# Performance work log

Hardware: AMD Instinct MI355X
Metric: run time of the kernel (lower is better)

The kernel has to match this reference:

```python
import jax, jax.numpy as jnp
import numpy as np

L, D, FF, H, S, B, W = 4, 768, 3072, 12, 4096, 4, 128


def setup_inputs() -> dict:
    key = jax.random.key(0)
    ks = jax.random.split(key, 8)
    w_ = lambda k, shape: jax.random.normal(k, shape, jnp.float32) * 0.02
    return {
        "x": jax.random.normal(ks[0], (B, S, D), jnp.float32),
        "Wq": w_(ks[1], (L, D, D)), "bq": jnp.zeros((L, D), jnp.float32),
        "Wk": w_(ks[2], (L, D, D)), "bk": jnp.zeros((L, D), jnp.float32),
        "Wv": w_(ks[3], (L, D, D)), "bv": jnp.zeros((L, D), jnp.float32),
        "W1": w_(ks[4], (L, D, FF)), "b1": jnp.zeros((L, FF), jnp.float32),
        "W2": w_(ks[5], (L, FF, D)), "b2": jnp.zeros((L, D), jnp.float32),
        "g1": jnp.ones((L, D), jnp.float32), "beta1": jnp.zeros((L, D), jnp.float32),
        "g2": jnp.ones((L, D), jnp.float32), "beta2": jnp.zeros((L, D), jnp.float32),
        "n_heads": H,
        "window": W,
    }


def _layernorm(x, g, b, eps=1e-5):
    m = jnp.mean(x, axis=-1, keepdims=True)
    v = jnp.mean(jnp.square(x - m), axis=-1, keepdims=True)
    return (x - m) * jax.lax.rsqrt(v + eps) * g + b


def _sliding_attn(x, Wq, bq, Wk, bk, Wv, bv, n_heads, w):
    # Longformer 'sliding_chunks' self-attention, one-sided window w (band 2w+1).
    b_, s_, d_ = x.shape
    hd = d_ // n_heads
    nc = s_ // w  # number of query chunks of size w

    def proj(Wm, bm):
        p = x @ Wm + bm
        return p.reshape(b_, s_, n_heads, hd).transpose(0, 2, 1, 3)  # [B,H,S,hd]

    q = proj(Wq, bq) / jnp.sqrt(jnp.asarray(hd, x.dtype))
    k = proj(Wk, bk)
    v = proj(Wv, bv)

    # pad keys/values by one window each side so every query chunk sees 3w keys
    kp = jnp.pad(k, ((0, 0), (0, 0), (w, w), (0, 0)))
    vp = jnp.pad(v, ((0, 0), (0, 0), (w, w), (0, 0)))
    idx = jnp.arange(nc)[:, None] * w + jnp.arange(3 * w)[None, :]  # [nc, 3w]
    kb = kp[:, :, idx]  # [B,H,nc,3w,hd]
    vb = vp[:, :, idx]
    qc = q.reshape(b_, n_heads, nc, w, hd)

    scores = jnp.einsum('bhcqd,bhckd->bhcqk', qc, kb)  # [B,H,nc,w,3w]

    # band + boundary mask: key pos = c*w + kj - w, query pos = c*w + qi
    c = jnp.arange(nc)[:, None, None]
    qi = jnp.arange(w)[None, :, None]
    kj = jnp.arange(3 * w)[None, None, :]
    rel = kj - qi - w
    kpos = c * w + kj - w
    mask = (jnp.abs(rel) <= w) & (kpos >= 0) & (kpos < s_)  # [nc,w,3w]

    scores = jnp.where(mask[None, None], scores, -jnp.inf)
    attn = jax.nn.softmax(scores, axis=-1)
    out = jnp.einsum('bhcqk,bhckd->bhcqd', attn, vb)  # [B,H,nc,w,hd]
    return out.reshape(b_, n_heads, s_, hd).transpose(0, 2, 1, 3).reshape(b_, s_, d_)


def reference(x, Wq, bq, Wk, bk, Wv, bv, W1, b1, W2, b2, g1, beta1, g2, beta2,
              n_heads, window):
    n_layers = Wq.shape[0]
    for l in range(n_layers):
        attn = _sliding_attn(x, Wq[l], bq[l], Wk[l], bk[l], Wv[l], bv[l],
                             n_heads, window)
        x = _layernorm(x + attn, g1[l], beta1[l])
        h = jnp.maximum(x @ W1[l] + b1[l], 0.0) @ W2[l] + b2[l]
        x = _layernorm(x + h, g2[l], beta2[l])
    return x
```

## Files before the change

kernel.cpp:

```cpp
#include <hip/hip_runtime.h>
#include <hip/hip_bf16.h>
#include <type_traits>

#define LAYERS 4
#define D      768
#define FF     3072
#define NH     12
#define HD     64
#define SEQ    4096
#define BATCH  4
#define WIN    128
#define NC     (SEQ / WIN)
#define NTOK   (BATCH * SEQ)

using bf16 = __hip_bfloat16;
typedef short short8 __attribute__((ext_vector_type(8)));
typedef short short4v __attribute__((ext_vector_type(4)));
typedef float floatx4 __attribute__((ext_vector_type(4)));

__device__ __forceinline__ float b2f(unsigned short u) {
    return __uint_as_float(((unsigned)u) << 16);
}
__device__ __forceinline__ short f2bs(float f) {
    union { bf16 h; short s; } u; u.h = __float2bfloat16(f); return u.s;
}
__device__ __forceinline__ void st_cvt(float* p, float v) { *p = v; }
__device__ __forceinline__ void st_cvt(bf16* p, float v) { *p = __float2bfloat16(v); }

__device__ __forceinline__ void gl_lds16(const void* g, void* l) {
    __builtin_amdgcn_global_load_lds(
        (const __attribute__((address_space(1))) void*)g,
        (__attribute__((address_space(3))) void*)l, 16, 0, 0);
}

__global__ __launch_bounds__(256)
void cvt_f32_bf16(const float* __restrict__ src, bf16* __restrict__ dst)
{
    const int i = (blockIdx.x * 256 + threadIdx.x) * 8;
    const float4 a0 = *(const float4*)(src + i);
    const float4 a1 = *(const float4*)(src + i + 4);
    short8 p = { f2bs(a0.x), f2bs(a0.y), f2bs(a0.z), f2bs(a0.w),
                 f2bs(a1.x), f2bs(a1.y), f2bs(a1.z), f2bs(a1.w) };
    *(short8*)((short*)dst + i) = p;
}

__global__ __launch_bounds__(256)
void transpose_cvt(const float* __restrict__ src, bf16* __restrict__ dst, int K, int N)
{
    __shared__ float t[32][33];
    const int n0 = blockIdx.x * 32, k0 = blockIdx.y * 32;
    const int tx = threadIdx.x & 31, ty = threadIdx.x >> 5;
    #pragma unroll
    for (int r = 0; r < 4; ++r)
        t[ty + 8 * r][tx] = src[(size_t)(k0 + ty + 8 * r) * N + n0 + tx];
    __syncthreads();
    #pragma unroll
    for (int r = 0; r < 4; ++r)
        dst[(size_t)(n0 + ty + 8 * r) * K + k0 + tx] = __float2bfloat16(t[tx][ty + 8 * r]);
}

template<int RELU, int OMODE, typename TC>
__global__ __launch_bounds__(256)
void mfma_gemm_bf(const bf16* __restrict__ A, const bf16* __restrict__ Wt,
                  const float* __restrict__ bias, TC* __restrict__ C,
                  int M, int N, int K, float scale)
{
    __shared__ __align__(16) short As[128 * 32];
    __shared__ __align__(16) short Bs[128 * 32];
    const int tid  = threadIdx.x;
    const int lane = tid & 63;
    const int wave = tid >> 6;
    const int quad = lane >> 4, l16 = lane & 15;
    const int mw = (wave >> 1) * 64, nw = (wave & 1) * 64;
    const int row0 = blockIdx.x * 128;
    const int col0 = blockIdx.y * 128;

    const unsigned short* Ag = (const unsigned short*)A;
    const unsigned short* Bg = (const unsigned short*)Wt;
    const int sr = lane >> 2;
    const int sc = (lane & 3) * 8;

    floatx4 acc[4][4];
    const floatx4 zero = {0.f, 0.f, 0.f, 0.f};
    #pragma unroll
    for (int i = 0; i < 4; ++i)
        #pragma unroll
        for (int j = 0; j < 4; ++j) acc[i][j] = zero;

    const size_t abase = (size_t)row0 * K;
    const size_t bbase = (size_t)col0 * K;

    for (int k0 = 0; k0 < K; k0 += 32) {
        __syncthreads();
        #pragma unroll
        for (int e = 0; e < 2; ++e) {
            const int seg = wave * 2 + e;
            const int r = seg * 16 + sr;
            gl_lds16(Ag + abase + (size_t)r * K + k0 + sc, &As[seg * 512]);
            gl_lds16(Bg + bbase + (size_t)r * K + k0 + sc, &Bs[seg * 512]);
        }
        __syncthreads();
        short8 af[4], bfr[4];
        #pragma unroll
        for (int i = 0; i < 4; ++i)
            af[i] = *(const short8*)&As[(mw + 16 * i + l16) * 32 + quad * 8];
        #pragma unroll
        for (int j = 0; j < 4; ++j)
            bfr[j] = *(const short8*)&Bs[(nw + 16 * j + l16) * 32 + quad * 8];
        #pragma unroll
        for (int i = 0; i < 4; ++i)
            #pragma unroll
            for (int j = 0; j < 4; ++j)
                acc[i][j] = __builtin_amdgcn_mfma_f32_16x16x32_bf16(af[i], bfr[j], acc[i][j], 0, 0, 0);
    }
    #pragma unroll
    for (int j = 0; j < 4; ++j) {
        const int c = col0 + nw + 16 * j + l16;
        const float bv = bias[c];
        #pragma unroll
        for (int i = 0; i < 4; ++i) {
            const int rr0 = row0 + mw + 16 * i + quad * 4;
            if constexpr (OMODE == 2) {
                short4v pack;
                #pragma unroll
                for (int r = 0; r < 4; ++r)
                    pack[r] = f2bs((acc[i][j][r] + bv) * scale);
                const int b_ = rr0 >> 12, s_ = rr0 & (SEQ - 1);
                const int h_ = c >> 6, d_ = c & (HD - 1);
                *(short4v*)&C[(((size_t)(b_ * NH + h_)) * HD + d_) * SEQ + s_] = pack;
            } else {
                #pragma unroll
                for (int r = 0; r < 4; ++r) {
                    float v = acc[i][j][r] + bv;
                    if (RELU) v = fmaxf(v, 0.f);
                    v *= scale;
                    const int rr = rr0 + r;
                    if constexpr (OMODE == 1) {
                        const int b_ = rr >> 12, s_ = rr & (SEQ - 1);
                        const int h_ = c >> 6, d_ = c & (HD - 1);
                        st_cvt(&C[(((size_t)(b_ * NH + h_)) * SEQ + s_) * HD + d_], v);
                    } else {
                        st_cvt(&C[(size_t)rr * N + c], v);
                    }
                }
            }
        }
    }
}

template<int RELU, int OMODE, typename TA, typename TC>
__global__ __launch_bounds__(256)
void mfma_gemm(const TA* __restrict__ A, const float* __restrict__ Wf,
               const float* __restrict__ bias,
               TC* __restrict__ C, int M, int N, int K, float scale)
{
    __shared__ __align__(16) short As[128][40];
    __shared__ __align__(16) short Bs[128][40];
    const int row0 = blockIdx.x * 128;
    const int col0 = blockIdx.y * 128;
    const int tid  = threadIdx.x;
    const int lane = tid & 63;
    const int wave = tid >> 6;
    const int quad = lane >> 4, l16 = lane & 15;
    const int mw = (wave >> 1) * 64, nw = (wave & 1) * 64;

    const int ar = tid >> 1;
    const int ah = (tid & 1) * 16;
    const int bn = tid & 127;
    const int bk = (tid >> 7) * 8;

    floatx4 acc[4][4];
    const floatx4 zero = {0.f, 0.f, 0.f, 0.f};
    #pragma unroll
    for (int i = 0; i < 4; ++i)
        #pragma unroll
        for (int j = 0; j < 4; ++j) acc[i][j] = zero;

    for (int k0 = 0; k0 < K; k0 += 32) {
        __syncthreads();
        if constexpr (std::is_same<TA, float>::value) {
            const float* ap = A + (size_t)(row0 + ar) * K + k0 + ah;
            float4 a0 = *(const float4*)(ap);
            float4 a1 = *(const float4*)(ap + 4);
            float4 a2 = *(const float4*)(ap + 8);
            float4 a3 = *(const float4*)(ap + 12);
            short8 p0 = { f2bs(a0.x), f2bs(a0.y), f2bs(a0.z), f2bs(a0.w),
                          f2bs(a1.x), f2bs(a1.y), f2bs(a1.z), f2bs(a1.w) };
            short8 p1 = { f2bs(a2.x), f2bs(a2.y), f2bs(a2.z), f2bs(a2.w),
                          f2bs(a3.x), f2bs(a3.y), f2bs(a3.z), f2bs(a3.w) };
            *(short8*)&As[ar][ah]     = p0;
            *(short8*)&As[ar][ah + 8] = p1;
        } else {
            const short* ap = (const short*)A + (size_t)(row0 + ar) * K + k0 + ah;
            *(short8*)&As[ar][ah]     = *(const short8*)(ap);
            *(short8*)&As[ar][ah + 8] = *(const short8*)(ap + 8);
        }
        #pragma unroll
        for (int kc = 0; kc < 2; ++kc) {
            const int kk = bk + kc * 16;
            short tmp[8];
            #pragma unroll
            for (int e = 0; e < 8; ++e)
                tmp[e] = f2bs(Wf[(size_t)(k0 + kk + e) * N + col0 + bn]);
            *(short8*)&Bs[bn][kk] = *(short8*)tmp;
        }
        __syncthreads();
        short8 af[4], bfr[4];
        #pragma unroll
        for (int i = 0; i < 4; ++i)
            af[i] = *(const short8*)&As[mw + 16 * i + l16][quad * 8];
        #pragma unroll
        for (int j = 0; j < 4; ++j)
            bfr[j] = *(const short8*)&Bs[nw + 16 * j + l16][quad * 8];
        #pragma unroll
        for (int i = 0; i < 4; ++i)
            #pragma unroll
            for (int j = 0; j < 4; ++j)
                acc[i][j] = __builtin_amdgcn_mfma_f32_16x16x32_bf16(af[i], bfr[j], acc[i][j], 0, 0, 0);
    }
    #pragma unroll
    for (int j = 0; j < 4; ++j) {
        const int c = col0 + nw + 16 * j + l16;
        const float bv = bias[c];
        #pragma unroll
        for (int i = 0; i < 4; ++i) {
            const int rr0 = row0 + mw + 16 * i + quad * 4;
            if constexpr (OMODE == 2) {
                short4v pack;
                #pragma unroll
                for (int r = 0; r < 4; ++r)
                    pack[r] = f2bs((acc[i][j][r] + bv) * scale);
                const int b_ = rr0 >> 12, s_ = rr0 & (SEQ - 1);
                const int h_ = c >> 6, d_ = c & (HD - 1);
                *(short4v*)&C[(((size_t)(b_ * NH + h_)) * HD + d_) * SEQ + s_] = pack;
            } else {
                #pragma unroll
                for (int r = 0; r < 4; ++r) {
                    float v = acc[i][j][r] + bv;
                    if (RELU) v = fmaxf(v, 0.f);
                    v *= scale;
                    const int rr = rr0 + r;
                    if constexpr (OMODE == 1) {
                        const int b_ = rr >> 12, s_ = rr & (SEQ - 1);
                        const int h_ = c >> 6, d_ = c & (HD - 1);
                        st_cvt(&C[(((size_t)(b_ * NH + h_)) * SEQ + s_) * HD + d_], v);
                    } else {
                        st_cvt(&C[(size_t)rr * N + c], v);
                    }
                }
            }
        }
    }
}

__global__ __launch_bounds__(256, 2)
void attn_mfma_kernel(const bf16* __restrict__ q, const bf16* __restrict__ k,
                      const bf16* __restrict__ v, bf16* __restrict__ out)
{
    __shared__ __align__(16) short Qs[128][72];
    __shared__ __align__(16) short Ks[64][72];
    __shared__ __align__(16) short Vs[64][72];
    __shared__ __align__(16) short Ps[4][32][72];

    const int c = blockIdx.x, h = blockIdx.y, b = blockIdx.z;
    const int tid = threadIdx.x;
    const int wave = tid >> 6, lane = tid & 63;
    const int quad = lane >> 4, l16 = lane & 15;
    const int qbase = wave * 32;

    const unsigned short* qg = (const unsigned short*)q + ((size_t)(b * NH + h)) * SEQ * HD;
    const unsigned short* kg = (const unsigned short*)k + ((size_t)(b * NH + h)) * SEQ * HD;
    const unsigned short* vg = (const unsigned short*)v + ((size_t)(b * NH + h)) * HD * SEQ;

    #pragma unroll
    for (int e = 0; e < 4; ++e) {
        const int idx = tid + e * 256;
        const int row = idx >> 3, d0 = (idx & 7) * 8;
        *(uint4*)&Qs[row][d0] = *(const uint4*)(qg + (size_t)(c * WIN + row) * HD + d0);
    }

    floatx4 O[2][4];
    const floatx4 zero = {0.f, 0.f, 0.f, 0.f};
    float m_i[2][4], l_i[2][4];
    #pragma unroll
    for (int i = 0; i < 2; ++i)
        #pragma unroll
        for (int r = 0; r < 4; ++r) { m_i[i][r] = -1e30f; l_i[i][r] = 0.f; }
    #pragma unroll
    for (int i = 0; i < 2; ++i)
        #pragma unroll
        for (int dj = 0; dj < 4; ++dj) O[i][dj] = zero;

    for (int sl = 0; sl < 6; ++sl) {
        const int s0 = sl * 64;
        const int kpos0 = c * WIN - WIN + s0;
        if (kpos0 < 0 || kpos0 >= SEQ) continue;
        __syncthreads();
        #pragma unroll
        for (int e = 0; e < 2; ++e) {
            const int idx = tid + e * 256;
            const int row = idx >> 3, d0 = (idx & 7) * 8;
            *(uint4*)&Ks[row][d0] = *(const uint4*)(kg + (size_t)(kpos0 + row) * HD + d0);
            *(uint4*)&Vs[row][d0] = *(const uint4*)(vg + (size_t)row * SEQ + kpos0 + d0);
        }
        __syncthreads();
        short8 aq[2][2], bk2[4][2];
        #pragma unroll
        for (int i = 0; i < 2; ++i)
            #pragma unroll
            for (int hh = 0; hh < 2; ++hh)
                aq[i][hh] = *(const short8*)&Qs[qbase + 16 * i + l16][hh * 32 + quad * 8];
        #pragma unroll
        for (int j = 0; j < 4; ++j)
            #pragma unroll
            for (int hh = 0; hh < 2; ++hh)
                bk2[j][hh] = *(const short8*)&Ks[16 * j + l16][hh * 32 + quad * 8];
        floatx4 sc[2][4];
        #pragma unroll
        for (int i = 0; i < 2; ++i)
            #pragma unroll
            for (int j = 0; j < 4; ++j) {
                floatx4 t = __builtin_amdgcn_mfma_f32_16x16x32_bf16(aq[i][0], bk2[j][0], zero, 0, 0, 0);
                sc[i][j]  = __builtin_amdgcn_mfma_f32_16x16x32_bf16(aq[i][1], bk2[j][1], t, 0, 0, 0);
            }
        #pragma unroll
        for (int i = 0; i < 2; ++i) {
            #pragma unroll
            for (int r = 0; r < 4; ++r) {
                const int qq = qbase + 16 * i + quad * 4 + r;
                float sv[4];
                float mx = -1e30f;
                #pragma unroll
                for (int j = 0; j < 4; ++j) {
                    const int kj = s0 + 16 * j + l16;
                    const bool ok = (kj >= qq) && (kj <= qq + 2 * WIN);
                    const float s = ok ? sc[i][j][r] : -1e30f;
                    sv[j] = s;
                    mx = fmaxf(mx, s);
                }
                mx = fmaxf(mx, __shfl_xor(mx, 1));
                mx = fmaxf(mx, __shfl_xor(mx, 2));
                mx = fmaxf(mx, __shfl_xor(mx, 4));
                mx = fmaxf(mx, __shfl_xor(mx, 8));
                const float mn = fmaxf(m_i[i][r], mx);
                const float corr = __expf(m_i[i][r] - mn);
                m_i[i][r] = mn;
                float ps = 0.f;
                #pragma unroll
                for (int j = 0; j < 4; ++j) {
                    const float p = (sv[j] > -0.9e30f) ? __expf(sv[j] - mn) : 0.f;
                    ps += p;
                    Ps[wave][16 * i + quad * 4 + r][16 * j + l16] = f2bs(p);
                }
                ps += __shfl_xor(ps, 1);
                ps += __shfl_xor(ps, 2);
                ps += __shfl_xor(ps, 4);
                ps += __shfl_xor(ps, 8);
                l_i[i][r] = l_i[i][r] * corr + ps;
                #pragma unroll
                for (int dj = 0; dj < 4; ++dj) O[i][dj][r] *= corr;
            }
        }
        short8 ap[2][2], bv2[4][2];
        #pragma unroll
        for (int i = 0; i < 2; ++i)
            #pragma unroll
            for (int hh = 0; hh < 2; ++hh)
                ap[i][hh] = *(const short8*)&Ps[wave][16 * i + l16][hh * 32 + quad * 8];
        #pragma unroll
        for (int dj = 0; dj < 4; ++dj)
            #pragma unroll
            for (int hh = 0; hh < 2; ++hh)
                bv2[dj][hh] = *(const short8*)&Vs[16 * dj + l16][hh * 32 + quad * 8];
        #pragma unroll
        for (int i = 0; i < 2; ++i)
            #pragma unroll
            for (int dj = 0; dj < 4; ++dj) {
                O[i][dj] = __builtin_amdgcn_mfma_f32_16x16x32_bf16(ap[i][0], bv2[dj][0], O[i][dj], 0, 0, 0);
                O[i][dj] = __builtin_amdgcn_mfma_f32_16x16x32_bf16(ap[i][1], bv2[dj][1], O[i][dj], 0, 0, 0);
            }
    }
    bf16* og = out + ((size_t)b * SEQ + c * WIN) * D + h * HD;
    #pragma unroll
    for (int i = 0; i < 2; ++i) {
        #pragma unroll
        for (int r = 0; r < 4; ++r) {
            const float inv = 1.f / l_i[i][r];
            const int qq = qbase + 16 * i + quad * 4 + r;
            #pragma unroll
            for (int dj = 0; dj < 4; ++dj)
                og[(size_t)qq * D + 16 * dj + l16] = __float2bfloat16(O[i][dj][r] * inv);
        }
    }
}

template<int WBF>
__global__ __launch_bounds__(256)
void add_ln_kernel(const float* __restrict__ xin, const bf16* __restrict__ h,
                   float* __restrict__ xout, bf16* __restrict__ xbf,
                   const float* __restrict__ g, const float* __restrict__ beta)
{
    const int row = blockIdx.x;
    __shared__ float buf[D];
    __shared__ float wsum[4], wsum2[4];
    const float* xr = xin + (size_t)row * D;
    const bf16* hr = h + (size_t)row * D;
    float s = 0.f, s2 = 0.f;
    #pragma unroll
    for (int e = 0; e < 3; ++e) {
        const int i = threadIdx.x + e * 256;
        const float t = xr[i] + __bfloat162float(hr[i]);
        buf[i] = t;
        s += t; s2 += t * t;
    }
    #pragma unroll
    for (int off = 32; off > 0; off >>= 1) {
        s  += __shfl_down(s, off);
        s2 += __shfl_down(s2, off);
    }
    const int wid = threadIdx.x >> 6, lane = threadIdx.x & 63;
    if (lane == 0) { wsum[wid] = s; wsum2[wid] = s2; }
    __syncthreads();
    if (threadIdx.x == 0) {
        const float S  = wsum[0] + wsum[1] + wsum[2] + wsum[3];
        const float S2 = wsum2[0] + wsum2[1] + wsum2[2] + wsum2[3];
        const float mean = S * (1.f / D);
        const float var  = S2 * (1.f / D) - mean * mean;
        wsum[0]  = mean;
        wsum2[0] = rsqrtf(var + 1e-5f);
    }
    __syncthreads();
    const float mean = wsum[0], inv = wsum2[0];
    #pragma unroll
    for (int e = 0; e < 3; ++e) {
        const int i = threadIdx.x + e * 256;
        const float val = (buf[i] - mean) * inv * g[i] + beta[i];
        xout[(size_t)row * D + i] = val;
        if constexpr (WBF)
            xbf[(size_t)row * D + i] = __float2bfloat16(val);
    }
}

static void run_fast(const float* x0,
                     const float* Wq, const float* bq, const float* Wk, const float* bk,
                     const float* Wv, const float* bv, const float* W1, const float* b1,
                     const float* W2, const float* b2, const float* g1, const float* be1,
                     const float* g2, const float* be2, float* out,
                     bf16* qb, bf16* kb, bf16* vb, bf16* hb, bf16* mid, bf16* h2,
                     bf16* wt, bf16* xbf, hipStream_t stream)
{
    const dim3 gD(NTOK / 128, D / 128);
    const dim3 gF(NTOK / 128, FF / 128);
    const dim3 ga(NC, NH, BATCH);
    const size_t DDm = (size_t)D * D, DFFm = (size_t)D * FF;

    cvt_f32_bf16<<<NTOK * D / 2048, 256, 0, stream>>>(x0, xbf);
    for (int l = 0; l < LAYERS; ++l) {
        const float* xin = (l == 0) ? x0 : out;
        transpose_cvt<<<dim3(D / 32, D / 32), 256, 0, stream>>>(
            Wq + (size_t)l * DDm, wt, D, D);
        transpose_cvt<<<dim3(D / 32, D / 32), 256, 0, stream>>>(
            Wk + (size_t)l * DDm, wt + DDm, D, D);
        transpose_cvt<<<dim3(D / 32, D / 32), 256, 0, stream>>>(
            Wv + (size_t)l * DDm, wt + 2 * DDm, D, D);
        transpose_cvt<<<dim3(FF / 32, D / 32), 256, 0, stream>>>(
            W1 + (size_t)l * DFFm, wt + 3 * DDm, D, FF);
        transpose_cvt<<<dim3(D / 32, FF / 32), 256, 0, stream>>>(
            W2 + (size_t)l * DFFm, wt + 3 * DDm + DFFm, FF, D);

        mfma_gemm_bf<0, 1, bf16><<<gD, 256, 0, stream>>>(
            xbf, wt, bq + (size_t)l * D, qb, NTOK, D, D, 0.125f);
        mfma_gemm_bf<0, 1, bf16><<<gD, 256, 0, stream>>>(
            xbf, wt + DDm, bk + (size_t)l * D, kb, NTOK, D, D, 1.0f);
        mfma_gemm_bf<0, 2, bf16><<<gD, 256, 0, stream>>>(
            xbf, wt + 2 * DDm, bv + (size_t)l * D, vb, NTOK, D, D, 1.0f);
        attn_mfma_kernel<<<ga, 256, 0, stream>>>(qb, kb, vb, hb);
        add_ln_kernel<1><<<NTOK, 256, 0, stream>>>(xin, hb, out, xbf,
            g1 + (size_t)l * D, be1 + (size_t)l * D);
        mfma_gemm_bf<1, 0, bf16><<<gF, 256, 0, stream>>>(
            xbf, wt + 3 * DDm, b1 + (size_t)l * FF, mid, NTOK, FF, D, 1.0f);
        mfma_gemm_bf<0, 0, bf16><<<gD, 256, 0, stream>>>(
            mid, wt + 3 * DDm + DFFm, b2 + (size_t)l * D, h2, NTOK, D, FF, 1.0f);
        add_ln_kernel<1><<<NTOK, 256, 0, stream>>>(out, h2, out, xbf,
            g2 + (size_t)l * D, be2 + (size_t)l * D);
    }
}

static void run_fallback(const float* x0,
                         const float* Wq, const float* bq, const float* Wk, const float* bk,
                         const float* Wv, const float* bv, const float* W1, const float* b1,
                         const float* W2, const float* b2, const float* g1, const float* be1,
                         const float* g2, const float* be2, float* out,
                         bf16* qb, bf16* kb, bf16* vb, bf16* hb, bf16* mid, bf16* h2,
                         hipStream_t stream)
{
    const dim3 gD(NTOK / 128, D / 128);
    const dim3 gF(NTOK / 128, FF / 128);
    const dim3 ga(NC, NH, BATCH);
    for (int l = 0; l < LAYERS; ++l) {
        const float* xin = (l == 0) ? x0 : out;
        mfma_gemm<0, 1, float, bf16><<<gD, 256, 0, stream>>>(
            xin, Wq + (size_t)l * D * D, bq + (size_t)l * D, qb, NTOK, D, D, 0.125f);
        mfma_gemm<0, 1, float, bf16><<<gD, 256, 0, stream>>>(
            xin, Wk + (size_t)l * D * D, bk + (size_t)l * D, kb, NTOK, D, D, 1.0f);
        mfma_gemm<0, 2, float, bf16><<<gD, 256, 0, stream>>>(
            xin, Wv + (size_t)l * D * D, bv + (size_t)l * D, vb, NTOK, D, D, 1.0f);
        attn_mfma_kernel<<<ga, 256, 0, stream>>>(qb, kb, vb, hb);
        add_ln_kernel<0><<<NTOK, 256, 0, stream>>>(xin, hb, out, nullptr,
            g1 + (size_t)l * D, be1 + (size_t)l * D);
        mfma_gemm<1, 0, float, bf16><<<gF, 256, 0, stream>>>(
            out, W1 + (size_t)l * D * FF, b1 + (size_t)l * FF, mid, NTOK, FF, D, 1.0f);
        mfma_gemm<0, 0, bf16, bf16><<<gD, 256, 0, stream>>>(
            mid, W2 + (size_t)l * FF * D, b2 + (size_t)l * D, h2, NTOK, D, FF, 1.0f);
        add_ln_kernel<0><<<NTOK, 256, 0, stream>>>(out, h2, out, nullptr,
            g2 + (size_t)l * D, be2 + (size_t)l * D);
    }
}

extern "C" void kernel_launch(void* const* d_in, const int* in_sizes, int n_in,
                              void* d_out, int out_size, void* d_ws, size_t ws_size,
                              hipStream_t stream)
{
    const float* x0  = (const float*)d_in[0];
    const float* Wq  = (const float*)d_in[1];
    const float* bq  = (const float*)d_in[2];
    const float* Wk  = (const float*)d_in[3];
    const float* bk  = (const float*)d_in[4];
    const float* Wv  = (const float*)d_in[5];
    const float* bv  = (const float*)d_in[6];
    const float* W1  = (const float*)d_in[7];
    const float* b1  = (const float*)d_in[8];
    const float* W2  = (const float*)d_in[9];
    const float* b2  = (const float*)d_in[10];
    const float* g1  = (const float*)d_in[11];
    const float* be1 = (const float*)d_in[12];
    const float* g2  = (const float*)d_in[13];
    const float* be2 = (const float*)d_in[14];
    float* out = (float*)d_out;

    const size_t QE = (size_t)BATCH * NH * SEQ * HD;
    const size_t LW = (size_t)3 * D * D + 2 * (size_t)D * FF;
    bf16* qb  = (bf16*)d_ws;
    bf16* kb  = qb + QE;
    bf16* vb  = kb + QE;
    bf16* hb  = vb + QE;
    bf16* mid = qb;
    bf16* h2  = qb + 4 * QE;
    bf16* wt  = qb + 5 * QE;
    bf16* xbf = wt + LW;
    const bool fast = ws_size >= (6 * QE + LW) * sizeof(bf16);

    if (fast) {
        run_fast(x0, Wq, bq, Wk, bk, Wv, bv, W1, b1, W2, b2, g1, be1, g2, be2,
                 out, qb, kb, vb, hb, mid, h2, wt, xbf, stream);
    } else {
        run_fallback(x0, Wq, bq, Wk, bk, Wv, bv, W1, b1, W2, b2, g1, be1, g2, be2,
                     out, qb, kb, vb, hb, mid, h2, stream);
    }
}
```

Measured before the change: 1.898 ms.

## Add 256x256 eight-wave pipelined GEMM with fused QKV projection

Replaces the 128x128 four-wave GEMMs with a new 256x256-tile, 512-thread kernel. It uses direct global-to-LDS loads into a swizzled, double-buffered 128KB LDS layout, interleaves MFMA and load phases with explicit barriers, waitcnts and priority hints, and remaps blocks for cache locality. The Q, K and V projections are merged into one launch with N=2304, and each output slice is routed with its own bias, scale and layout. The aim is higher MFMA utilisation and fewer launches, at the cost of a large LDS footprint per block and a fragile hand-tuned schedule.

```diff
diff --git a/kernel.cpp b/kernel.cpp
--- a/kernel.cpp
+++ b/kernel.cpp
@@ -33,6 +33,14 @@
         (__attribute__((address_space(3))) void*)l, 16, 0, 0);
 }
 
+#define SB0   __builtin_amdgcn_sched_barrier(0)
+#define BAR   __builtin_amdgcn_s_barrier()
+#define LGKM0 asm volatile("s_waitcnt lgkmcnt(0)" ::: "memory")
+#define VM4   asm volatile("s_waitcnt vmcnt(4)" ::: "memory")
+#define VM0   asm volatile("s_waitcnt vmcnt(0)" ::: "memory")
+#define SP1   __builtin_amdgcn_s_setprio(1)
+#define SP0   __builtin_amdgcn_s_setprio(0)
+
 __global__ __launch_bounds__(256)
 void cvt_f32_bf16(const float* __restrict__ src, bf16* __restrict__ dst)
 {
@@ -59,10 +67,175 @@
         dst[(size_t)(n0 + ty + 8 * r) * K + k0 + tx] = __float2bfloat16(t[tx][ty + 8 * r]);
 }
 
-template<int RELU, int OMODE, typename TC>
+template<int OMODE, int RELU>
+__global__ __launch_bounds__(512, 2)
+void gemm8(const bf16* __restrict__ A, const bf16* __restrict__ Wt,
+           const float* __restrict__ b0, const float* __restrict__ b1p,
+           const float* __restrict__ b2p, bf16* __restrict__ C,
+           int K, int N)
+{
+    extern __shared__ char ldsc[];
+    const int tid  = threadIdx.x;
+    const int lane = tid & 63;
+    const int wave = tid >> 6;
+    const int quad = lane >> 4, l16 = lane & 15;
+    const int wm = wave >> 2, wn = wave & 3;
+
+    const int bx  = blockIdx.x;
+    const int bxs = (bx & 7) * 8 + (bx >> 3);
+    const int row0 = bxs * 256;
+    const int col0 = blockIdx.y * 256;
+
+    const int lin0 = wave * 1024 + lane * 16;
+    const int lin1 = 8192 + wave * 1024 + lane * 16;
+    const int rl0 = lin0 >> 7, rl1 = lin1 >> 7;
+    const int so0 = (lin0 & 127) ^ ((rl0 & 7) << 4);
+    const int so1 = (lin1 & 127) ^ ((rl1 & 7) << 4);
+    const char* agl0 = (const char*)A  + 2 * ((size_t)(row0 + rl0) * K) + so0;
+    const char* agl1 = (const char*)A  + 2 * ((size_t)(row0 + rl1) * K) + so1;
+    const char* bgl0 = (const char*)Wt + 2 * ((size_t)(col0 + rl0) * K) + so0;
+    const char* bgl1 = (const char*)Wt + 2 * ((size_t)(col0 + rl1) * K) + so1;
+    const size_t hstr = (size_t)128 * K * 2;
+
+#define STA(d,h,kt) do { \
+    gl_lds16(agl0 + ((h) ? hstr : 0) + (size_t)(kt) * 128, ldsc + ((d)*2+(h))*16384 + lin0); \
+    gl_lds16(agl1 + ((h) ? hstr : 0) + (size_t)(kt) * 128, ldsc + ((d)*2+(h))*16384 + lin1); } while (0)
+#define STB(d,h,kt) do { \
+    gl_lds16(bgl0 + ((h) ? hstr : 0) + (size_t)(kt) * 128, ldsc + 65536 + ((d)*2+(h))*16384 + lin0); \
+    gl_lds16(bgl1 + ((h) ? hstr : 0) + (size_t)(kt) * 128, ldsc + 65536 + ((d)*2+(h))*16384 + lin1); } while (0)
+
+    const int arow  = wm * 64 + l16;
+    const int abase = arow * 128;
+    const int sA    = (arow & 7) << 4;
+    const int aof0  = (quad * 16) ^ sA;
+    const int aof1  = (64 + quad * 16) ^ sA;
+    const int brow  = wn * 32 + l16;
+    const int bbase = brow * 128;
+    const int sB    = (brow & 7) << 4;
+    const int bof0  = (quad * 16) ^ sB;
+    const int bof1  = (64 + quad * 16) ^ sB;
+
+    short8 af[4][2], bf0[2][2], bf1[2][2];
+    floatx4 acc[2][2][4][2];
+    const floatx4 zero = {0.f, 0.f, 0.f, 0.f};
+    #pragma unroll
+    for (int a = 0; a < 2; ++a)
+        #pragma unroll
+        for (int b = 0; b < 2; ++b)
+            #pragma unroll
+            for (int m = 0; m < 4; ++m)
+                #pragma unroll
+                for (int n = 0; n < 2; ++n) acc[a][b][m][n] = zero;
+
+#define LDA(slot) do { const char* ab_ = ldsc + (slot)*16384 + abase; \
+    _Pragma("unroll") for (int m_ = 0; m_ < 4; ++m_) { \
+        af[m_][0] = *(const short8*)(ab_ + m_*2048 + aof0); \
+        af[m_][1] = *(const short8*)(ab_ + m_*2048 + aof1); } } while (0)
+#define LDB(slot, BF) do { const char* bb_ = ldsc + 65536 + (slot)*16384 + bbase; \
+    _Pragma("unroll") for (int n_ = 0; n_ < 2; ++n_) { \
+        BF[n_][0] = *(const short8*)(bb_ + n_*2048 + bof0); \
+        BF[n_][1] = *(const short8*)(bb_ + n_*2048 + bof1); } } while (0)
+#define MM(mh, nh, BF) do { \
+    _Pragma("unroll") for (int m_ = 0; m_ < 4; ++m_) \
+    _Pragma("unroll") for (int n_ = 0; n_ < 2; ++n_) { \
+        acc[mh][nh][m_][n_] = __builtin_amdgcn_mfma_f32_16x16x32_bf16(af[m_][0], BF[n_][0], acc[mh][nh][m_][n_], 0, 0, 0); \
+        acc[mh][nh][m_][n_] = __builtin_amdgcn_mfma_f32_16x16x32_bf16(af[m_][1], BF[n_][1], acc[mh][nh][m_][n_], 0, 0, 0); } } while (0)
+
+    const int nkt   = K >> 6;
+    const int niter = K >> 7;
+
+    STA(0,0,0); STB(0,0,0); STA(0,1,0); STB(0,1,0);
+    STA(1,0,1); STB(1,0,1);
+    VM4; SB0; BAR;
+
+    for (int i = 0; i < niter; ++i) {
+        const int k1 = 2*i + 1;
+        const int k2 = (2*i + 2 < nkt) ? 2*i + 2 : nkt - 1;
+        const int k3 = (2*i + 3 < nkt) ? 2*i + 3 : nkt - 1;
+        LDA(0); LDB(0, bf0); STA(1,1,k1); SB0; BAR; LGKM0; SB0;
+        SP1; MM(0,0,bf0); SP0; SB0; BAR;
+        LDB(1, bf1); STB(1,1,k1); SB0; BAR; LGKM0; SB0;
+        SP1; MM(0,1,bf1); SP0; SB0; BAR;
+        LDA(1); STA(0,0,k2); SB0; BAR; LGKM0; SB0;
+        SP1; MM(1,0,bf0); SP0; SB0; BAR;
+        STB(0,0,k2); SB0; BAR; LGKM0; SB0;
+        SP1; MM(1,1,bf1); SP0; VM4; SB0; BAR;
+        LDA(2); LDB(2, bf0); STA(0,1,k2); SB0; BAR; LGKM0; SB0;
+        SP1; MM(0,0,bf0); SP0; SB0; BAR;
+        LDB(3, bf1); STB(0,1,k2); SB0; BAR; LGKM0; SB0;
+        SP1; MM(0,1,bf1); SP0; SB0; BAR;
+        LDA(3); STA(1,0,k3); SB0; BAR; LGKM0; SB0;
+        SP1; MM(1,0,bf0); SP0; SB0; BAR;
+        STB(1,0,k3); SB0; BAR; LGKM0; SB0;
+        SP1; MM(1,1,bf1); SP0; VM4; SB0; BAR;
+    }
+    VM0;
+
+#undef STA
+#undef STB
+#undef LDA
+#undef LDB
+#undef MM
+
+    constexpr size_t QEc = (size_t)BATCH * NH * SEQ * HD;
+    int sel = 0;
+    const float* bptr = b0;
+    float scl = 1.0f;
+    int ccb = col0;
+    if constexpr (OMODE == 3) {
+        sel  = blockIdx.y / 3;
+        bptr = (sel == 0) ? b0 : (sel == 1) ? b1p : b2p;
+        scl  = (sel == 0) ? 0.125f : 1.0f;
+        ccb  = col0 - sel * 768;
+    }
+    #pragma unroll
+    for (int mh = 0; mh < 2; ++mh)
+    #pragma unroll
+    for (int nh = 0; nh < 2; ++nh)
+    #pragma unroll
+    for (int n = 0; n < 2; ++n) {
+        const int c  = ccb + nh * 128 + wn * 32 + n * 16 + l16;
+        const float bvv = bptr[c];
+        #pragma unroll
+        for (int m = 0; m < 4; ++m) {
+            const int rr0 = row0 + mh * 128 + wm * 64 + m * 16 + quad * 4;
+            if constexpr (OMODE == 3) {
+                if (sel == 2) {
+                    short4v pack;
+                    #pragma unroll
+                    for (int r = 0; r < 4; ++r)
+                        pack[r] = f2bs(acc[mh][nh][m][n][r] + bvv);
+                    const int b_ = rr0 >> 12, s_ = rr0 & (SEQ - 1);
+                    const int h_ = c >> 6, d_ = c & (HD - 1);
+                    bf16* Cv = C + 2 * QEc;
+                    *(short4v*)&Cv[(((size_t)(b_ * NH + h_)) * HD + d_) * SEQ + s_] = pack;
+                } else {
+                    bf16* Cq = C + (size_t)sel * QEc;
+                    #pragma unroll
+                    for (int r = 0; r < 4; ++r) {
+                        const float v = (acc[mh][nh][m][n][r] + bvv) * scl;
+                        const int rr = rr0 + r;
+                        const int b_ = rr >> 12, s_ = rr & (SEQ - 1);
+                        const int h_ = c >> 6, d_ = c & (HD - 1);
+                        Cq[(((size_t)(b_ * NH + h_)) * SEQ + s_) * HD + d_] = __float2bfloat16(v);
+                    }
+                }
+            } else {
+                #pragma unroll
+                for (int r = 0; r < 4; ++r) {
+                    float v = acc[mh][nh][m][n][r] + bvv;
+                    if (RELU) v = fmaxf(v, 0.f);
+                    C[(size_t)(rr0 + r) * N + c] = __float2bfloat16(v);
+                }
+            }
+        }
+    }
+}
+
+template<int RELU, int OMODE>
 __global__ __launch_bounds__(256)
 void mfma_gemm_bf(const bf16* __restrict__ A, const bf16* __restrict__ Wt,
-                  const float* __restrict__ bias, TC* __restrict__ C,
+                  const float* __restrict__ bias, bf16* __restrict__ C,
                   int M, int N, int K, float scale)
 {
     __shared__ __align__(16) short As[128 * 32];
@@ -441,18 +614,20 @@
     }
 }
 
-static void run_fast(const float* x0,
-                     const float* Wq, const float* bq, const float* Wk, const float* bk,
-                     const float* Wv, const float* bv, const float* W1, const float* b1,
-                     const float* W2, const float* b2, const float* g1, const float* be1,
-                     const float* g2, const float* be2, float* out,
-                     bf16* qb, bf16* kb, bf16* vb, bf16* hb, bf16* mid, bf16* h2,
-                     bf16* wt, bf16* xbf, hipStream_t stream)
-{
-    const dim3 gD(NTOK / 128, D / 128);
-    const dim3 gF(NTOK / 128, FF / 128);
+static void run_fast8(const float* x0,
+                      const float* Wq, const float* bq, const float* Wk, const float* bk,
+                      const float* Wv, const float* bv, const float* W1, const float* b1,
+                      const float* W2, const float* b2, const float* g1, const float* be1,
+                      const float* g2, const float* be2, float* out,
+                      bf16* qb, bf16* kb, bf16* vb, bf16* hb, bf16* mid, bf16* h2,
+                      bf16* wt, bf16* xbf, hipStream_t stream)
+{
+    const dim3 gQKV(64, 9);
+    const dim3 gF1(64, 12);
+    const dim3 gF2(64, 3);
     const dim3 ga(NC, NH, BATCH);
     const size_t DDm = (size_t)D * D, DFFm = (size_t)D * FF;
+    const int SMEM = 131072;
 
     cvt_f32_bf16<<<NTOK * D / 2048, 256, 0, stream>>>(x0, xbf);
     for (int l = 0; l < LAYERS; ++l) {
@@ -468,18 +643,62 @@
         transpose_cvt<<<dim3(D / 32, FF / 32), 256, 0, stream>>>(
             W2 + (size_t)l * DFFm, wt + 3 * DDm + DFFm, FF, D);
 
-        mfma_gemm_bf<0, 1, bf16><<<gD, 256, 0, stream>>>(
+        gemm8<3, 0><<<gQKV, 512, SMEM, stream>>>(
+            xbf, wt, bq + (size_t)l * D, bk + (size_t)l * D, bv + (size_t)l * D,
+            qb, D, 2304);
+        attn_mfma_kernel<<<ga, 256, 0, stream>>>(qb, kb, vb, hb);
+        add_ln_kernel<1><<<NTOK, 256, 0, stream>>>(xin, hb, out, xbf,
+            g1 + (size_t)l * D, be1 + (size_t)l * D);
+        gemm8<0, 1><<<gF1, 512, SMEM, stream>>>(
+            xbf, wt + 3 * DDm, b1 + (size_t)l * FF, nullptr, nullptr,
+            mid, D, FF);
+        gemm8<0, 0><<<gF2, 512, SMEM, stream>>>(
+            mid, wt + 3 * DDm + DFFm, b2 + (size_t)l * D, nullptr, nullptr,
+            h2, FF, D);
+        add_ln_kernel<1><<<NTOK, 256, 0, stream>>>(out, h2, out, xbf,
+            g2 + (size_t)l * D, be2 + (size_t)l * D);
+    }
+}
+
+static void run_fast_old(const float* x0,
+                         const float* Wq, const float* bq, const float* Wk, const float* bk,
+                         const float* Wv, const float* bv, const float* W1, const float* b1,
+                         const float* W2, const float* b2, const float* g1, const float* be1,
+                         const float* g2, const float* be2, float* out,
+                         bf16* qb, bf16* kb, bf16* vb, bf16* hb, bf16* mid, bf16* h2,
+                         bf16* wt, bf16* xbf, hipStream_t stream)
+{
+    const dim3 gD(NTOK / 128, D / 128);
+    const dim3 gF(NTOK / 128, FF / 128);
+    const dim3 ga(NC, NH, BATCH);
+    const size_t DDm = (size_t)D * D, DFFm = (size_t)D * FF;
+
+    cvt_f32_bf16<<<NTOK * D / 2048, 256, 0, stream>>>(x0, xbf);
+    for (int l = 0; l < LAYERS; ++l) {
+        const float* xin = (l == 0) ? x0 : out;
+        transpose_cvt<<<dim3(D / 32, D / 32), 256, 0, stream>>>(
+            Wq + (size_t)l * DDm, wt, D, D);
+        transpose_cvt<<<dim3(D / 32, D / 32), 256, 0, stream>>>(
+            Wk + (size_t)l * DDm, wt + DDm, D, D);
+        transpose_cvt<<<dim3(D / 32, D / 32), 256, 0, stream>>>(
+            Wv + (size_t)l * DDm, wt + 2 * DDm, D, D);
+        transpose_cvt<<<dim3(FF / 32, D / 32), 256, 0, stream>>>(
+            W1 + (size_t)l * DFFm, wt + 3 * DDm, D, FF);
+        transpose_cvt<<<dim3(D / 32, FF / 32), 256, 0, stream>>>(
+            W2 + (size_t)l * DFFm, wt + 3 * DDm + DFFm, FF, D);
+
+        mfma_gemm_bf<0, 1><<<gD, 256, 0, stream>>>(
             xbf, wt, bq + (size_t)l * D, qb, NTOK, D, D, 0.125f);
-        mfma_gemm_bf<0, 1, bf16><<<gD, 256, 0, stream>>>(
+        mfma_gemm_bf<0, 1><<<gD, 256, 0, stream>>>(
             xbf, wt + DDm, bk + (size_t)l * D, kb, NTOK, D, D, 1.0f);
-        mfma_gemm_bf<0, 2, bf16><<<gD, 256, 0, stream>>>(
+        mfma_gemm_bf<0, 2><<<gD, 256, 0, stream>>>(
             xbf, wt + 2 * DDm, bv + (size_t)l * D, vb, NTOK, D, D, 1.0f);
         attn_mfma_kernel<<<ga, 256, 0, stream>>>(qb, kb, vb, hb);
         add_ln_kernel<1><<<NTOK, 256, 0, stream>>>(xin, hb, out, xbf,
             g1 + (size_t)l * D, be1 + (size_t)l * D);
-        mfma_gemm_bf<1, 0, bf16><<<gF, 256, 0, stream>>>(
+        mfma_gemm_bf<1, 0><<<gF, 256, 0, stream>>>(
             xbf, wt + 3 * DDm, b1 + (size_t)l * FF, mid, NTOK, FF, D, 1.0f);
-        mfma_gemm_bf<0, 0, bf16><<<gD, 256, 0, stream>>>(
+        mfma_gemm_bf<0, 0><<<gD, 256, 0, stream>>>(
             mid, wt + 3 * DDm + DFFm, b2 + (size_t)l * D, h2, NTOK, D, FF, 1.0f);
         add_ln_kernel<1><<<NTOK, 256, 0, stream>>>(out, h2, out, xbf,
             g2 + (size_t)l * D, be2 + (size_t)l * D);
@@ -550,9 +769,24 @@
     bf16* xbf = wt + LW;
     const bool fast = ws_size >= (6 * QE + LW) * sizeof(bf16);
 
-    if (fast) {
-        run_fast(x0, Wq, bq, Wk, bk, Wv, bv, W1, b1, W2, b2, g1, be1, g2, be2,
-                 out, qb, kb, vb, hb, mid, h2, wt, xbf, stream);
+    static int attr_state = 0;
+    if (attr_state == 0) {
+        bool ok = true;
+        ok &= hipFuncSetAttribute((const void*)(gemm8<3, 0>),
+              hipFuncAttributeMaxDynamicSharedMemorySize, 131072) == hipSuccess;
+        ok &= hipFuncSetAttribute((const void*)(gemm8<0, 1>),
+              hipFuncAttributeMaxDynamicSharedMemorySize, 131072) == hipSuccess;
+        ok &= hipFuncSetAttribute((const void*)(gemm8<0, 0>),
+              hipFuncAttributeMaxDynamicSharedMemorySize, 131072) == hipSuccess;
+        attr_state = ok ? 1 : -1;
+    }
+
+    if (fast && attr_state == 1) {
+        run_fast8(x0, Wq, bq, Wk, bk, Wv, bv, W1, b1, W2, b2, g1, be1, g2, be2,
+                  out, qb, kb, vb, hb, mid, h2, wt, xbf, stream);
+    } else if (fast) {
+        run_fast_old(x0, Wq, bq, Wk, bk, Wv, bv, W1, b1, W2, b2, g1, be1, g2, be2,
+                     out, qb, kb, vb, hb, mid, h2, wt, xbf, stream);
     } else {
         run_fallback(x0, Wq, bq, Wk, bk, Wv, bv, W1, b1, W2, b2, g1, be1, g2, be2,
                      out, qb, kb, vb, hb, mid, h2, stream);
```

Measured after the change: 1.652 ms. -13.0%, faster.
